# Performance work log

Hardware: AMD Instinct MI355X
Metric: run time of the kernel (lower is better)

Reference implementation:

```python
import jax, jax.numpy as jnp
import numpy as np

TWO_PI = 2.0 * np.pi
MIN_W = 1e-3
MIN_H = 1e-3
MIN_D = 1e-3
DERIV_SHIFT = float(np.log(np.e - 1.0))  # softplus(x+shift)=1 at x=0


def setup_inputs() -> dict:
    key = jax.random.key(0)
    k0, k1, k2, k3 = jax.random.split(key, 4)
    B, C, H, K, Dh = 131072, 64, 256, 32, 8
    theta = jax.random.uniform(k0, (B, Dh), dtype=jnp.float32) * (TWO_PI * 0.999)
    x_conditioner = jax.random.normal(k1, (B, C), dtype=jnp.float32)
    W1 = jax.random.normal(k2, (C, H), dtype=jnp.float32) / np.sqrt(C)
    b1 = jnp.zeros((H,), jnp.float32)
    W2 = jax.random.normal(k3, (H, 3 * K * Dh), dtype=jnp.float32) / np.sqrt(H)
    b2 = jnp.zeros((3 * K * Dh,), jnp.float32)
    eta = jnp.ones((1,), jnp.float32)
    return dict(theta=theta, x_conditioner=x_conditioner, W1=W1, b1=b1, W2=W2, b2=b2, eta=eta)


def _gather(knots, idx):
    # knots: (..., K'), idx: (...) -> (...)
    return jnp.take_along_axis(knots, idx[..., None], axis=-1)[..., 0]


def _circular_rq_spline_fwd(inputs, uw, uh, ud):
    # inputs: (B, Dh) in [0, 2pi); uw/uh/ud: (B, Dh, K)
    K = uw.shape[-1]
    # circular derivatives: pad with first element so d[0] == d[K]
    ud = jnp.concatenate([ud, ud[..., :1]], axis=-1)  # (B, Dh, K+1)
    derivatives = MIN_D + jax.nn.softplus(ud)

    widths = MIN_W + (1.0 - MIN_W * K) * jax.nn.softmax(uw, axis=-1)
    cumwidths = jnp.cumsum(widths, axis=-1)
    cumwidths = jnp.pad(cumwidths, [(0, 0)] * (cumwidths.ndim - 1) + [(1, 0)])
    cumwidths = TWO_PI * cumwidths
    cumwidths = cumwidths.at[..., 0].set(0.0).at[..., -1].set(TWO_PI)
    widths = cumwidths[..., 1:] - cumwidths[..., :-1]

    heights = MIN_H + (1.0 - MIN_H * K) * jax.nn.softmax(uh, axis=-1)
    cumheights = jnp.cumsum(heights, axis=-1)
    cumheights = jnp.pad(cumheights, [(0, 0)] * (cumheights.ndim - 1) + [(1, 0)])
    cumheights = TWO_PI * cumheights
    cumheights = cumheights.at[..., 0].set(0.0).at[..., -1].set(TWO_PI)
    heights = cumheights[..., 1:] - cumheights[..., :-1]

    delta = heights / widths  # (B, Dh, K)

    # bin search (nflows-style searchsorted)
    idx = jnp.sum(inputs[..., None] >= cumwidths, axis=-1) - 1
    idx = jnp.clip(idx, 0, K - 1)

    in_cumw = _gather(cumwidths, idx)
    in_w = _gather(widths, idx)
    in_cumh = _gather(cumheights, idx)
    in_h = _gather(heights, idx)
    in_delta = _gather(delta, idx)
    in_d = _gather(derivatives, idx)
    in_d1 = _gather(derivatives[..., 1:], idx)

    t = (inputs - in_cumw) / in_w
    t1mt = t * (1.0 - t)
    numerator = in_h * (in_delta * t * t + in_d * t1mt)
    denominator = in_delta + (in_d + in_d1 - 2.0 * in_delta) * t1mt
    outputs = in_cumh + numerator / denominator

    deriv_num = in_delta * in_delta * (in_d1 * t * t + 2.0 * in_delta * t1mt + in_d * (1.0 - t) ** 2)
    logabsdet = jnp.log(deriv_num) - 2.0 * jnp.log(denominator)
    return outputs, logabsdet


def reference(theta, x_conditioner, W1, b1, W2, b2, eta):
    B, Dh = theta.shape
    K = W2.shape[-1] // (3 * Dh)
    h = jax.nn.relu(x_conditioner @ W1 + b1)
    params = (h @ W2 + b2) * eta[0]
    params = params.reshape(B, Dh, 3 * K)
    uw, uh, ud = jnp.split(params, 3, axis=-1)
    ud = ud + DERIV_SHIFT
    return _circular_rq_spline_fwd(theta, uw, uh, ud)
```

## Files before the change

kernel.cpp:

```cpp
#include <hip/hip_runtime.h>
#include <hip/hip_bf16.h>
#include <math.h>

#define B_TOTAL   131072
#define C_IN      64
#define H_DIM     256
#define K_KNOTS   32
#define DH        8
#define P_DIM     768
#define R_ROWS    64
#define NTHREADS  512

#define TWO_PI_F       6.2831853071795864769f
#define MIN_WF         1e-3f
#define MIN_HF         1e-3f
#define MIN_DF         1e-3f
#define DERIV_SHIFT_F  0.54132485461292f

typedef __attribute__((ext_vector_type(8))) short bf16x8;
typedef __attribute__((ext_vector_type(4))) float f32x4;

#define SXH_BYTE  0
#define SXL_BYTE  8192
#define SHH_BYTE  16384
#define SHL_BYTE  49152
#define LDS_BYTES 99840

#define W2P_ELEMS 196608
#define W1P_ELEMS 16384

__device__ __forceinline__ short f2bf(float x) {
    __hip_bfloat16 h = __float2bfloat16(x);
    return *reinterpret_cast<short*>(&h);
}
__device__ __forceinline__ float bf2f(short s) {
    unsigned u = ((unsigned)(unsigned short)s) << 16;
    return __uint_as_float(u);
}

__device__ __forceinline__ float softplus_f(float x) {
    return (x > 15.f) ? x : log1pf(__expf(x));
}

__global__ __launch_bounds__(256)
void pack_weights(const float* __restrict__ W1, const float* __restrict__ W2,
                  short* __restrict__ W1p_hi, short* __restrict__ W1p_lo,
                  short* __restrict__ W2p_hi, short* __restrict__ W2p_lo)
{
    const int idx = blockIdx.x * 256 + threadIdx.x;
    if (idx < W2P_ELEMS) {
        const int j  = idx & 7;
        const int l  = (idx >> 3) & 63;
        const int c  = idx >> 9;
        const int kc = c & 7;
        const int nt = c >> 3;
        const int k  = kc * 32 + (l >> 4) * 8 + j;
        const int n  = nt * 16 + (l & 15);
        const float wv = W2[k * P_DIM + n];
        const short hi = f2bf(wv);
        W2p_hi[idx] = hi;
        W2p_lo[idx] = f2bf(wv - bf2f(hi));
    } else {
        const int i2 = idx - W2P_ELEMS;
        if (i2 < W1P_ELEMS) {
            const int j  = i2 & 7;
            const int l  = (i2 >> 3) & 63;
            const int c  = i2 >> 9;
            const int kc = c & 1;
            const int nt = c >> 1;
            const int k  = kc * 32 + (l >> 4) * 8 + j;
            const int n  = nt * 16 + (l & 15);
            const float wv = W1[k * H_DIM + n];
            const short hi = f2bf(wv);
            W1p_hi[i2] = hi;
            W1p_lo[i2] = f2bf(wv - bf2f(hi));
        }
    }
}

__global__ __launch_bounds__(NTHREADS, 1)
void spline_mfma(const float* __restrict__ theta,
                 const float* __restrict__ X,
                 const short* __restrict__ W1p_hi,
                 const short* __restrict__ W1p_lo,
                 const float* __restrict__ b1,
                 const short* __restrict__ W2p_hi,
                 const short* __restrict__ W2p_lo,
                 const float* __restrict__ b2,
                 const float* __restrict__ eta,
                 float* __restrict__ out)
{
    extern __shared__ float smem[];
    char*  sXh = reinterpret_cast<char*>(smem) + SXH_BYTE;
    char*  sXl = reinterpret_cast<char*>(smem) + SXL_BYTE;
    char*  sHh = reinterpret_cast<char*>(smem) + SHH_BYTE;
    char*  sHl = reinterpret_cast<char*>(smem) + SHL_BYTE;
    float* sP  = smem;

    const int t    = threadIdx.x;
    const int r0   = blockIdx.x * R_ROWS;
    const int lane = t & 63;
    const int w    = t >> 6;

    #pragma unroll
    for (int i = 0; i < 2; ++i) {
        const int idx = t + i * NTHREADS;
        const float4 v = reinterpret_cast<const float4*>(X + (size_t)r0 * C_IN)[idx];
        const int row = idx >> 4;
        const int c0  = (idx & 15) * 4;
        const int slot = c0 >> 3;
        const int byte = row * 128 + ((slot ^ (row & 7)) << 4) + ((c0 & 4) << 1);
        short4 hv, lv;
        hv.x = f2bf(v.x); lv.x = f2bf(v.x - bf2f(hv.x));
        hv.y = f2bf(v.y); lv.y = f2bf(v.y - bf2f(hv.y));
        hv.z = f2bf(v.z); lv.z = f2bf(v.z - bf2f(hv.z));
        hv.w = f2bf(v.w); lv.w = f2bf(v.w - bf2f(hv.w));
        *reinterpret_cast<short4*>(sXh + byte) = hv;
        *reinterpret_cast<short4*>(sXl + byte) = lv;
    }
    __syncthreads();

    {
        f32x4 acc[4][2] = {};
        #pragma unroll
        for (int kc = 0; kc < 2; ++kc) {
            bf16x8 ah[4], al[4];
            #pragma unroll
            for (int mt = 0; mt < 4; ++mt) {
                const int arow = mt * 16 + (lane & 15);
                const int aslot = kc * 4 + (lane >> 4);
                const int off = arow * 128 + ((aslot ^ (arow & 7)) << 4);
                ah[mt] = *reinterpret_cast<const bf16x8*>(sXh + off);
                al[mt] = *reinterpret_cast<const bf16x8*>(sXl + off);
            }
            #pragma unroll
            for (int ntl = 0; ntl < 2; ++ntl) {
                const int nt = 2 * w + ntl;
                const int boff = ((nt * 2 + kc) * 64 + lane) << 3;
                const bf16x8 bh = *reinterpret_cast<const bf16x8*>(W1p_hi + boff);
                const bf16x8 bl = *reinterpret_cast<const bf16x8*>(W1p_lo + boff);
                #pragma unroll
                for (int mt = 0; mt < 4; ++mt) {
                    acc[mt][ntl] = __builtin_amdgcn_mfma_f32_16x16x32_bf16(ah[mt], bh, acc[mt][ntl], 0, 0, 0);
                    acc[mt][ntl] = __builtin_amdgcn_mfma_f32_16x16x32_bf16(ah[mt], bl, acc[mt][ntl], 0, 0, 0);
                    acc[mt][ntl] = __builtin_amdgcn_mfma_f32_16x16x32_bf16(al[mt], bh, acc[mt][ntl], 0, 0, 0);
                }
            }
        }
        #pragma unroll
        for (int ntl = 0; ntl < 2; ++ntl) {
            const int col  = (2 * w + ntl) * 16 + (lane & 15);
            const float bias = b1[col];
            #pragma unroll
            for (int mt = 0; mt < 4; ++mt) {
                #pragma unroll
                for (int r = 0; r < 4; ++r) {
                    const int row = mt * 16 + (lane >> 4) * 4 + r;
                    float h = acc[mt][ntl][r] + bias;
                    h = h > 0.f ? h : 0.f;
                    const int byte = row * 512 + ((((col >> 3) ^ (row & 7)) << 4)) + ((col & 7) * 2);
                    const short hh = f2bf(h);
                    *reinterpret_cast<short*>(sHh + byte) = hh;
                    *reinterpret_cast<short*>(sHl + byte) = f2bf(h - bf2f(hh));
                }
            }
        }
    }
    __syncthreads();

    f32x4 acc2[4][6] = {};
    {
        const int ntbase = w * 6;
        #pragma unroll
        for (int kc = 0; kc < 8; ++kc) {
            bf16x8 ah[4], al[4];
            #pragma unroll
            for (int mt = 0; mt < 4; ++mt) {
                const int arow = mt * 16 + (lane & 15);
                const int aslot = kc * 4 + (lane >> 4);
                const int off = arow * 512 + ((aslot ^ (arow & 7)) << 4);
                ah[mt] = *reinterpret_cast<const bf16x8*>(sHh + off);
                al[mt] = *reinterpret_cast<const bf16x8*>(sHl + off);
            }
            #pragma unroll
            for (int ntl = 0; ntl < 6; ++ntl) {
                const int nt = ntbase + ntl;
                const int boff = ((nt * 8 + kc) * 64 + lane) << 3;
                const bf16x8 bh = *reinterpret_cast<const bf16x8*>(W2p_hi + boff);
                const bf16x8 bl = *reinterpret_cast<const bf16x8*>(W2p_lo + boff);
                #pragma unroll
                for (int mt = 0; mt < 4; ++mt) {
                    acc2[mt][ntl] = __builtin_amdgcn_mfma_f32_16x16x32_bf16(ah[mt], bh, acc2[mt][ntl], 0, 0, 0);
                    acc2[mt][ntl] = __builtin_amdgcn_mfma_f32_16x16x32_bf16(ah[mt], bl, acc2[mt][ntl], 0, 0, 0);
                    acc2[mt][ntl] = __builtin_amdgcn_mfma_f32_16x16x32_bf16(al[mt], bh, acc2[mt][ntl], 0, 0, 0);
                }
            }
        }
    }
    const float ev = eta[0];
    __syncthreads();

    #pragma unroll
    for (int hp = 0; hp < 2; ++hp) {
        {
            const int ntbase = w * 6;
            #pragma unroll
            for (int ntl = 0; ntl < 6; ++ntl) {
                const int col = (ntbase + ntl) * 16 + (lane & 15);
                const int dh  = col / 96;
                const int j   = col - dh * 96;
                const float bias = b2[col];
                #pragma unroll
                for (int mtl = 0; mtl < 2; ++mtl) {
                    const int mt = hp * 2 + mtl;
                    #pragma unroll
                    for (int r = 0; r < 4; ++r) {
                        const int rowl = mtl * 16 + (lane >> 4) * 4 + r;
                        sP[rowl * 780 + dh * 97 + j] = (acc2[mt][ntl][r] + bias) * ev;
                    }
                }
            }
        }
        __syncthreads();

        if (t < 256) {
            const int rowl = t >> 3;
            const int dh   = t & 7;
            const float* p = &sP[rowl * 780 + dh * 97];
            const int gi = (r0 + hp * 32 + rowl) * DH + dh;
            const float th = theta[gi];

            float ew[K_KNOTS], eh[K_KNOTS];
            float mw = -1e30f, mh = -1e30f;
            #pragma unroll
            for (int k = 0; k < K_KNOTS; ++k) {
                ew[k] = p[k];
                eh[k] = p[32 + k];
                mw = fmaxf(mw, ew[k]);
                mh = fmaxf(mh, eh[k]);
            }
            float sw = 0.f, sh = 0.f;
            #pragma unroll
            for (int k = 0; k < K_KNOTS; ++k) {
                ew[k] = __expf(ew[k] - mw);
                eh[k] = __expf(eh[k] - mh);
                sw += ew[k];
                sh += eh[k];
            }
            const float scw = (1.f - MIN_WF * (float)K_KNOTS) / sw;
            const float sch = (1.f - MIN_HF * (float)K_KNOTS) / sh;

            float pw = 0.f, ph = 0.f;
            float cumw = 0.f, cumh = 0.f;
            float in_cumw = 0.f, in_w = 1.f, in_cumh = 0.f, in_h = 1.f;
            int idx = 0;
            #pragma unroll
            for (int k = 0; k < K_KNOTS; ++k) {
                pw += MIN_WF + ew[k] * scw;
                ph += MIN_HF + eh[k] * sch;
                const float cumw1 = (k == K_KNOTS - 1) ? TWO_PI_F : TWO_PI_F * pw;
                const float cumh1 = (k == K_KNOTS - 1) ? TWO_PI_F : TWO_PI_F * ph;
                if (th >= cumw) {
                    idx = k;
                    in_cumw = cumw; in_w = cumw1 - cumw;
                    in_cumh = cumh; in_h = cumh1 - cumh;
                }
                cumw = cumw1; cumh = cumh1;
            }

            const float ud0 = p[64 + idx] + DERIV_SHIFT_F;
            const int idx1 = (idx + 1) & (K_KNOTS - 1);
            const float ud1 = p[64 + idx1] + DERIV_SHIFT_F;
            const float in_d  = MIN_DF + softplus_f(ud0);
            const float in_d1 = MIN_DF + softplus_f(ud1);

            const float tt    = (th - in_cumw) / in_w;
            const float t1mt  = tt * (1.f - tt);
            const float delta = in_h / in_w;
            const float num   = in_h * (delta * tt * tt + in_d * t1mt);
            const float den   = delta + (in_d + in_d1 - 2.f * delta) * t1mt;
            const float outv  = in_cumh + num / den;
            const float omt   = 1.f - tt;
            const float dnum  = delta * delta * (in_d1 * tt * tt + 2.f * delta * t1mt + in_d * omt * omt);
            const float lad   = __logf(dnum) - 2.f * __logf(den);

            out[gi]                = outv;
            out[B_TOTAL * DH + gi] = lad;
        }
        __syncthreads();
    }
}

extern "C" void kernel_launch(void* const* d_in, const int* in_sizes, int n_in,
                              void* d_out, int out_size, void* d_ws, size_t ws_size,
                              hipStream_t stream) {
    const float* theta = (const float*)d_in[0];
    const float* X     = (const float*)d_in[1];
    const float* W1    = (const float*)d_in[2];
    const float* b1    = (const float*)d_in[3];
    const float* W2    = (const float*)d_in[4];
    const float* b2    = (const float*)d_in[5];
    const float* eta   = (const float*)d_in[6];
    float* out = (float*)d_out;

    short* W2p_hi = (short*)d_ws;
    short* W2p_lo = W2p_hi + W2P_ELEMS;
    short* W1p_hi = W2p_lo + W2P_ELEMS;
    short* W1p_lo = W1p_hi + W1P_ELEMS;

    pack_weights<<<(W2P_ELEMS + W1P_ELEMS) / 256, 256, 0, stream>>>(
        W1, W2, W1p_hi, W1p_lo, W2p_hi, W2p_lo);

    (void)hipFuncSetAttribute((const void*)spline_mfma,
                              hipFuncAttributeMaxDynamicSharedMemorySize,
                              LDS_BYTES);
    const int blocks = B_TOTAL / R_ROWS;
    spline_mfma<<<blocks, NTHREADS, LDS_BYTES, stream>>>(
        theta, X, W1p_hi, W1p_lo, b1, W2p_hi, W2p_lo, b2, eta, out);
}
```

Before: 259.7 us.

## Shrink LDS staging and register arrays to raise spline kernel occupancy

Splits the epilogue into four 16-row passes instead of two 32-row passes, which shrinks the LDS footprint and lets launch bounds request four blocks per CU. The per-thread exp arrays are dropped in favour of rolled loops that recompute exp from LDS, and the b2 bias loads are hoisted into registers. The goal is more waves resident to hide latency, at the cost of extra exp work, more barriers, and only 128 threads active in each spline pass.

Result: slower. 616.6 us (+137.5%).

```diff
diff --git a/kernel.cpp b/kernel.cpp
--- a/kernel.cpp
+++ b/kernel.cpp
@@ -24,7 +24,7 @@
 #define SXL_BYTE  8192
 #define SHH_BYTE  16384
 #define SHL_BYTE  49152
-#define LDS_BYTES 99840
+#define LDS_BYTES 81920
 
 #define W2P_ELEMS 196608
 #define W1P_ELEMS 16384
@@ -78,7 +78,7 @@
     }
 }
 
-__global__ __launch_bounds__(NTHREADS, 1)
+__global__ __launch_bounds__(NTHREADS, 4)
 void spline_mfma(const float* __restrict__ theta,
                  const float* __restrict__ X,
                  const short* __restrict__ W1p_hi,
@@ -198,54 +198,47 @@
         }
     }
     const float ev = eta[0];
+    float bias2[6];
+    #pragma unroll
+    for (int ntl = 0; ntl < 6; ++ntl)
+        bias2[ntl] = b2[(w * 6 + ntl) * 16 + (lane & 15)];
     __syncthreads();
 
     #pragma unroll
-    for (int hp = 0; hp < 2; ++hp) {
+    for (int hp = 0; hp < 4; ++hp) {
         {
-            const int ntbase = w * 6;
             #pragma unroll
             for (int ntl = 0; ntl < 6; ++ntl) {
-                const int col = (ntbase + ntl) * 16 + (lane & 15);
-                const int dh  = col / 96;
+                const int col = (w * 6 + ntl) * 16 + (lane & 15);
+                const int dh  = w;
                 const int j   = col - dh * 96;
-                const float bias = b2[col];
                 #pragma unroll
-                for (int mtl = 0; mtl < 2; ++mtl) {
-                    const int mt = hp * 2 + mtl;
-                    #pragma unroll
-                    for (int r = 0; r < 4; ++r) {
-                        const int rowl = mtl * 16 + (lane >> 4) * 4 + r;
-                        sP[rowl * 780 + dh * 97 + j] = (acc2[mt][ntl][r] + bias) * ev;
-                    }
+                for (int r = 0; r < 4; ++r) {
+                    const int rowl = (lane >> 4) * 4 + r;
+                    sP[rowl * 780 + dh * 97 + j] = (acc2[hp][ntl][r] + bias2[ntl]) * ev;
                 }
             }
         }
         __syncthreads();
 
-        if (t < 256) {
+        if (t < 128) {
             const int rowl = t >> 3;
             const int dh   = t & 7;
             const float* p = &sP[rowl * 780 + dh * 97];
-            const int gi = (r0 + hp * 32 + rowl) * DH + dh;
+            const int gi = (r0 + hp * 16 + rowl) * DH + dh;
             const float th = theta[gi];
 
-            float ew[K_KNOTS], eh[K_KNOTS];
             float mw = -1e30f, mh = -1e30f;
-            #pragma unroll
+            #pragma unroll 1
             for (int k = 0; k < K_KNOTS; ++k) {
-                ew[k] = p[k];
-                eh[k] = p[32 + k];
-                mw = fmaxf(mw, ew[k]);
-                mh = fmaxf(mh, eh[k]);
+                mw = fmaxf(mw, p[k]);
+                mh = fmaxf(mh, p[32 + k]);
             }
             float sw = 0.f, sh = 0.f;
-            #pragma unroll
+            #pragma unroll 1
             for (int k = 0; k < K_KNOTS; ++k) {
-                ew[k] = __expf(ew[k] - mw);
-                eh[k] = __expf(eh[k] - mh);
-                sw += ew[k];
-                sh += eh[k];
+                sw += __expf(p[k] - mw);
+                sh += __expf(p[32 + k] - mh);
             }
             const float scw = (1.f - MIN_WF * (float)K_KNOTS) / sw;
             const float sch = (1.f - MIN_HF * (float)K_KNOTS) / sh;
@@ -254,10 +247,10 @@
             float cumw = 0.f, cumh = 0.f;
             float in_cumw = 0.f, in_w = 1.f, in_cumh = 0.f, in_h = 1.f;
             int idx = 0;
-            #pragma unroll
+            #pragma unroll 1
             for (int k = 0; k < K_KNOTS; ++k) {
-                pw += MIN_WF + ew[k] * scw;
-                ph += MIN_HF + eh[k] * sch;
+                pw += MIN_WF + __expf(p[k] - mw) * scw;
+                ph += MIN_HF + __expf(p[32 + k] - mh) * sch;
                 const float cumw1 = (k == K_KNOTS - 1) ? TWO_PI_F : TWO_PI_F * pw;
                 const float cumh1 = (k == K_KNOTS - 1) ? TWO_PI_F : TWO_PI_F * ph;
                 if (th >= cumw) {
```
